# Performance work log

Measured on AMD Instinct MI355X. Metric: run time of the kernel, lower is better.

The kernel has to match this reference:

```python
import jax, jax.numpy as jnp
import numpy as np

XBOUND = (-30.0, 30.0, 0.25)
YBOUND = (-15.0, 15.0, 0.25)
ZBOUND = (-1.0, 1.0, 0.5)
EPS = 1e-9


def _heights():
    n = int((ZBOUND[1] - ZBOUND[0]) // ZBOUND[2]) + 1
    return [ZBOUND[0] + i * ZBOUND[2] for i in range(n)]


def _bev_planes():
    # matches construct_plane_grid: linspace endpoints included, meshgrid(y, x) 'ij'
    num_x = int((XBOUND[1] - XBOUND[0]) / XBOUND[2])
    num_y = int((YBOUND[1] - YBOUND[0]) / YBOUND[2])
    x = jnp.linspace(XBOUND[0], XBOUND[1], num_x, dtype=jnp.float32)
    y = jnp.linspace(YBOUND[0], YBOUND[1], num_y, dtype=jnp.float32)
    yy, xx = jnp.meshgrid(y, x, indexing='ij')
    planes = [jnp.stack([xx, yy, jnp.full_like(xx, h)], axis=-1) for h in _heights()]
    return jnp.stack(planes)  # (nlvl, bH, bW, 3)


def _bilinear_grid_sample(im, grid):
    # faithful port of the manual pad+floor+gather grid_sample (align_corners=False)
    n, c, h, w = im.shape
    gh, gw = grid.shape[1], grid.shape[2]
    x = ((grid[..., 0] + 1) * w - 1) / 2
    y = ((grid[..., 1] + 1) * h - 1) / 2
    x = x.reshape(n, -1)
    y = y.reshape(n, -1)
    x0 = jnp.floor(x)
    y0 = jnp.floor(y)
    wa = ((x0 + 1 - x) * (y0 + 1 - y))[:, None, :]
    wb = ((x0 + 1 - x) * (y - y0))[:, None, :]
    wc = ((x - x0) * (y0 + 1 - y))[:, None, :]
    wd = ((x - x0) * (y - y0))[:, None, :]
    pw, ph = w + 2, h + 2
    # clip in float first to avoid int32 overflow; out-of-range lands on zero padding either way
    x0f = jnp.clip(x0, -2.0, w + 2.0)
    y0f = jnp.clip(y0, -2.0, h + 2.0)
    x0i = jnp.clip(x0f.astype(jnp.int32) + 1, 0, pw - 1)
    x1i = jnp.clip(x0f.astype(jnp.int32) + 2, 0, pw - 1)
    y0i = jnp.clip(y0f.astype(jnp.int32) + 1, 0, ph - 1)
    y1i = jnp.clip(y0f.astype(jnp.int32) + 2, 0, ph - 1)
    im_flat = jnp.pad(im, ((0, 0), (0, 0), (1, 1), (1, 1))).reshape(n, c, -1)

    def gather(xi, yi):
        return jnp.take_along_axis(im_flat, (xi + yi * pw)[:, None, :], axis=2)

    out = (gather(x0i, y0i) * wa + gather(x0i, y1i) * wb
           + gather(x1i, y0i) * wc + gather(x1i, y1i) * wd)
    return out.reshape(n, c, gh, gw)


def _campos(pts, ego2cam, img_h, img_w):
    # pts: (B, q, 3); ego2cam: (B, ncam, 4, 4)
    B, q, _ = pts.shape
    ncam = ego2cam.shape[1]
    pts_h = jnp.concatenate([pts, jnp.ones_like(pts[..., :1])], axis=-1)  # (B,q,4)
    cam = jnp.einsum('bnij,bqj->bnqi', ego2cam, pts_h)  # (B,ncam,q,4)
    z = cam[..., 2:3]
    mask = z > EPS
    xy = cam[..., 0:2] / z + EPS
    px = xy[..., 0:1] / img_w
    py = xy[..., 1:2] / img_h
    p = (jnp.concatenate([px, py], axis=-1) - 0.5) * 2
    mask = (mask & (p[..., 0:1] > -1.0) & (p[..., 0:1] < 1.0)
            & (p[..., 1:2] > -1.0) & (p[..., 1:2] < 1.0))
    return p.reshape(B * ncam, q, 2), mask.reshape(B, ncam, q)


def reference(cam_feat, ego2cam, conv_w, conv_b, img_h, img_w):
    B, ncam = ego2cam.shape[0], ego2cam.shape[1]
    C = cam_feat.shape[1]
    planes = _bev_planes().astype(cam_feat.dtype)  # (nlvl,bH,bW,3)
    nlvl, bH, bW, _ = planes.shape
    pts = jnp.broadcast_to(planes.reshape(1, -1, 3), (B, nlvl * bH * bW, 3))
    pos, mask = _campos(pts, ego2cam, img_h, img_w)
    grid = pos.reshape(B * ncam, nlvl * bH, bW, 2)
    proj = _bilinear_grid_sample(cam_feat, grid).reshape(B, ncam, C, nlvl, bH, bW)
    m = mask.reshape(B, ncam, 1, nlvl, bH, bW).astype(proj.dtype)
    feat = (proj * m).sum(axis=1)            # (B,C,nlvl,bH,bW)
    num = m.sum(axis=1)                      # (B,1,nlvl,bH,bW)
    feat = feat / jnp.where(num == 0, jnp.ones_like(num), num)
    coords = jnp.broadcast_to(jnp.transpose(planes, (3, 0, 1, 2))[None], (B, 3, nlvl, bH, bW))
    feat = jnp.concatenate([feat, coords], axis=1).reshape(B, (C + 3) * nlvl, bH, bW)
    out = jax.lax.conv_general_dilated(
        feat, conv_w, window_strides=(1, 1), padding=((1, 1), (1, 1)),
        dimension_numbers=('NCHW', 'OIHW', 'NCHW'))
    return out + conv_b[None, :, None, None]


def setup_inputs() -> dict:
    key = jax.random.key(0)
    k1, k2, k3 = jax.random.split(key, 3)
    B, ncam, C = 1, 6, 128
    cH, cW = 64, 176
    nlvl = 5
    cam_feat = jax.random.normal(k1, (B * ncam, C, cH, cW), dtype=jnp.float32)
    ego2cam = jax.random.normal(k2, (B, ncam, 4, 4), dtype=jnp.float32)
    conv_w = jax.random.normal(k3, (128, (C + 3) * nlvl, 3, 3), dtype=jnp.float32) * 0.02
    conv_b = jnp.zeros((128,), dtype=jnp.float32)
    return {'cam_feat': cam_feat, 'ego2cam': ego2cam, 'conv_w': conv_w,
            'conv_b': conv_b, 'img_h': 512, 'img_w': 1408}
```

## Files before the change

### kernel.cpp

```cpp
#include <hip/hip_runtime.h>
#include <hip/hip_bf16.h>

#define BH 120
#define BW 240
#define NLVL 5
#define NCAM 6
#define CH 128
#define FH 64
#define FW 176
#define CIN 655
#define CINP 672
#define NCT 21
#define FROWS 124
#define FCOLS 242
#define NPIX (BH*BW)

typedef __hip_bfloat16 bf16;
typedef __attribute__((ext_vector_type(8))) short s16x8;
typedef __attribute__((ext_vector_type(4))) float f32x4;

#define G_AS __attribute__((address_space(1)))
#define L_AS __attribute__((address_space(3)))

__device__ __forceinline__ float bf2f(unsigned short u) {
    union { unsigned int i; float f; } c; c.i = ((unsigned int)u) << 16; return c.f;
}

__global__ __launch_bounds__(256) void transpose_kernel(
    const float* __restrict__ in, float* __restrict__ out)
{
    __shared__ float t[32][129];
    int n = blockIdx.z, h = blockIdx.y, w0 = blockIdx.x * 32;
    int wlim = min(32, FW - w0);
    int wx = threadIdx.x & 31, cg = threadIdx.x >> 5;
    if (wx < wlim) {
        #pragma unroll
        for (int k = 0; k < 16; ++k) {
            int c = cg + k * 8;
            t[wx][c] = in[((n*CH + c)*FH + h)*FW + w0 + wx];
        }
    }
    __syncthreads();
    int c2 = threadIdx.x & 127, wi = threadIdx.x >> 7;
    for (int w = wi; w < wlim; w += 2)
        out[((n*FH + h)*FW + w0 + w)*CH + c2] = t[w][c2];
}

__global__ __launch_bounds__(256) void wprep_kernel(
    const float* __restrict__ w, bf16* __restrict__ wbf)
{
    int idx = blockIdx.x * 256 + threadIdx.x;
    if (idx >= 128 * CINP) return;
    int oc = idx / CINP, cin = idx - oc * CINP;
    float v[9];
    if (cin < CIN) {
        const float* s = w + ((size_t)oc * CIN + cin) * 9;
        #pragma unroll
        for (int k = 0; k < 9; ++k) v[k] = s[k];
    } else {
        #pragma unroll
        for (int k = 0; k < 9; ++k) v[k] = 0.f;
    }
    #pragma unroll
    for (int k = 0; k < 9; ++k)
        wbf[(size_t)(k * 128 + oc) * CINP + cin] = __float2bfloat16(v[k]);
}

__global__ __launch_bounds__(128) void border_kernel(bf16* __restrict__ feat)
{
    int b = blockIdx.x;
    int row, col;
    if (b < 242)      { row = 0;   col = b; }
    else if (b < 484) { row = 121; col = b - 242; }
    else if (b < 604) { row = b - 484 + 1; col = 0; }
    else              { row = b - 604 + 1; col = 241; }
    s16x8* p = (s16x8*)(feat + ((size_t)row*FCOLS + col)*CINP);
    int t = threadIdx.x;
    if (t < 84) p[t] = (s16x8){0,0,0,0,0,0,0,0};
}

__global__ __launch_bounds__(128) void proj_kernel(
    const float* __restrict__ camt,
    const float* __restrict__ e2c,
    const int* __restrict__ pimgh, const int* __restrict__ pimgw,
    bf16* __restrict__ feat)
{
    __shared__ float sfx[30], sfy[30];
    __shared__ int   six[30], siy[30], svalid[30];

    int pix = blockIdx.x;
    int bx = pix % BW, by = pix / BW;
    float xw = (float)(-30.0 + bx * (60.0/239.0)); if (bx == BW-1) xw = 30.f;
    float yw = (float)(-15.0 + by * (30.0/119.0)); if (by == BH-1) yw = 15.f;

    int t = threadIdx.x;
    if (t < 30) {
        int l = t / 6, cam = t % 6;
        float h = -1.f + 0.5f * (float)l;
        const float* M = e2c + cam * 16;
        float cx = M[0]*xw + M[1]*yw + M[2]*h  + M[3];
        float cy = M[4]*xw + M[5]*yw + M[6]*h  + M[7];
        float cz = M[8]*xw + M[9]*yw + M[10]*h + M[11];
        float fw = (float)pimgw[0], fh = (float)pimgh[0];
        float px = ((cx/cz + 1e-9f)/fw - 0.5f) * 2.f;
        float py = ((cy/cz + 1e-9f)/fh - 0.5f) * 2.f;
        bool valid = (cz > 1e-9f) && (px > -1.f) && (px < 1.f)
                                  && (py > -1.f) && (py < 1.f);
        float xs = ((px + 1.f)*(float)FW - 1.f) * 0.5f;
        float ys = ((py + 1.f)*(float)FH - 1.f) * 0.5f;
        float x0 = floorf(xs), y0 = floorf(ys);
        sfx[t] = xs - x0;  sfy[t] = ys - y0;
        six[t] = (int)x0;  siy[t] = (int)y0;
        svalid[t] = valid ? 1 : 0;
    }
    __syncthreads();

    int c = t;
    float vals[NLVL];
    #pragma unroll
    for (int l = 0; l < NLVL; ++l) {
        float acc = 0.f; int cnt = 0;
        #pragma unroll
        for (int cam = 0; cam < NCAM; ++cam) {
            int id = l*6 + cam;
            if (svalid[id]) {
                int ix = six[id], iy = siy[id];
                float fx = sfx[id], fy = sfy[id];
                const float* bp = camt + (((size_t)cam*FH + iy)*FW + ix)*CH + c;
                float v00 = (ix >= 0    && iy >= 0   ) ? bp[0]        : 0.f;
                float v01 = (ix >= 0    && iy <  FH-1) ? bp[FW*CH]    : 0.f;
                float v10 = (ix <  FW-1 && iy >= 0   ) ? bp[CH]       : 0.f;
                float v11 = (ix <  FW-1 && iy <  FH-1) ? bp[FW*CH+CH] : 0.f;
                acc += (1.f-fx)*(1.f-fy)*v00 + (1.f-fx)*fy*v01
                     +      fx *(1.f-fy)*v10 +      fx *fy*v11;
                cnt++;
            }
        }
        vals[l] = acc / (float)(cnt > 0 ? cnt : 1);
    }

    bf16* dst = feat + ((size_t)(by+1)*FCOLS + (bx+1))*CINP;
    #pragma unroll
    for (int l = 0; l < NLVL; ++l)
        dst[c*5 + l] = __float2bfloat16(vals[l]);
    if (t < 15) {
        int j = t / 5, l = t % 5;
        float v = (j == 0) ? xw : (j == 1) ? yw : (-1.f + 0.5f*(float)l);
        dst[(CH + j)*5 + l] = __float2bfloat16(v);
    }
}

__global__ __launch_bounds__(256, 4) void conv_mfma_kernel(
    const bf16* __restrict__ feat,
    const bf16* __restrict__ wbf,
    bf16* __restrict__ part)
{
    __shared__ __align__(16) char lds[40960];
    const int tid  = threadIdx.x;
    const int wv   = tid >> 6;
    const int lane = tid & 63;
    const int t15  = tid & 15;
    const int kgl  = (tid >> 4) & 3;
    const int y0p = blockIdx.y * 8;
    const int x0p = blockIdx.x * 16;
    const int q   = blockIdx.z;
    const int ct0 = q ? (1 + 5*q) : 0;
    const int nph = (q ? 5 : 6) * 9;

    const int HB0 = 0, HB1 = 12288, WB0 = 24576, WB1 = 32768;

    f32x4 acc[8][2];
    #pragma unroll
    for (int m = 0; m < 8; ++m)
        #pragma unroll
        for (int f = 0; f < 2; ++f)
            acc[m][f] = (f32x4){0.f, 0.f, 0.f, 0.f};

    auto stageW = [&](int ct, int off, int wb) {
        #pragma unroll
        for (int jj = 0; jj < 2; ++jj) {
            int j = 2*wv + jj;
            int cch = j*64 + lane;
            int oc = cch >> 2, kgp = cch & 3;
            int kg = kgp ^ ((oc >> 1) & 3);
            const bf16* src = wbf + ((size_t)(off*128 + oc)*CINP + ct*32 + kg*8);
            __builtin_amdgcn_global_load_lds((const G_AS void*)src,
                                             (L_AS void*)(lds + wb + j*1024),
                                             16, 0, 0);
        }
    };
    auto stageH = [&](int ct, int hb) {
        #pragma unroll
        for (int kk = 0; kk < 3; ++kk) {
            int j = wv + 4*kk;
            int cch = j*64 + lane;
            int pp = cch >> 2, kgp = cch & 3;
            int kg = kgp ^ ((pp >> 1) & 3);
            int row = pp / 18;
            int col = pp - row*18;
            const bf16* src = feat + ((size_t)(y0p + row)*FCOLS + (x0p + col))*CINP
                                   + ct*32 + kg*8;
            __builtin_amdgcn_global_load_lds((const G_AS void*)src,
                                             (L_AS void*)(lds + hb + j*1024),
                                             16, 0, 0);
        }
    };

    stageH(ct0, HB0);
    stageW(ct0, 0, WB0);
    __syncthreads();

    int lct = 0, off = 0;
    for (int p = 0; p < nph; ++p) {
        if (p + 1 < nph) {
            int off1 = off + 1, lct1 = lct;
            if (off1 == 9) { off1 = 0; ++lct1; }
            stageW(ct0 + lct1, off1, ((p+1) & 1) ? WB1 : WB0);
            if (off1 == 0) stageH(ct0 + lct1, (lct1 & 1) ? HB1 : HB0);
        }
        const int wb = (p & 1) ? WB1 : WB0;
        const int hb = (lct & 1) ? HB1 : HB0;
        const int ky = off / 3, kx = off - ky*3;

        s16x8 A[8];
        #pragma unroll
        for (int m = 0; m < 8; ++m) {
            int oc = m*16 + t15;
            A[m] = *(const s16x8*)(lds + wb + oc*64 + ((kgl ^ ((oc>>1)&3)) << 4));
        }
        #pragma unroll
        for (int f = 0; f < 2; ++f) {
            int prow = (2*wv + f + ky)*18 + t15 + kx;
            s16x8 Bv = *(const s16x8*)(lds + hb + prow*64 + ((kgl ^ ((prow>>1)&3)) << 4));
            __builtin_amdgcn_s_setprio(1);
            #pragma unroll
            for (int m = 0; m < 8; ++m)
                acc[m][f] = __builtin_amdgcn_mfma_f32_16x16x32_bf16(A[m], Bv, acc[m][f], 0, 0, 0);
            __builtin_amdgcn_s_setprio(0);
        }
        __syncthreads();
        if (++off == 9) { off = 0; ++lct; }
    }

    bf16* pq = part + (size_t)q * (128*NPIX);
    const int xo = x0p + t15;
    #pragma unroll
    for (int m = 0; m < 8; ++m) {
        #pragma unroll
        for (int r = 0; r < 4; ++r) {
            int oc = m*16 + kgl*4 + r;
            #pragma unroll
            for (int f = 0; f < 2; ++f) {
                int y = y0p + 2*wv + f;
                pq[(size_t)oc*NPIX + y*BW + xo] = __float2bfloat16(acc[m][f][r]);
            }
        }
    }
}

__global__ __launch_bounds__(256) void combine_kernel(
    const bf16* __restrict__ part, const float* __restrict__ bias,
    float* __restrict__ out)
{
    int i8 = blockIdx.x * 256 + threadIdx.x;
    if (i8 >= 128*NPIX/8) return;
    int oc = i8 / (NPIX/8);
    float s[8];
    float b = bias[oc];
    #pragma unroll
    for (int k = 0; k < 8; ++k) s[k] = b;
    #pragma unroll
    for (int qq = 0; qq < 4; ++qq) {
        s16x8 v = *(const s16x8*)(part + (size_t)qq*(128*NPIX) + (size_t)i8*8);
        #pragma unroll
        for (int k = 0; k < 8; ++k) s[k] += bf2f((unsigned short)v[k]);
    }
    f32x4* o = (f32x4*)(out + (size_t)i8*8);
    o[0] = (f32x4){s[0], s[1], s[2], s[3]};
    o[1] = (f32x4){s[4], s[5], s[6], s[7]};
}

extern "C" void kernel_launch(void* const* d_in, const int* in_sizes, int n_in,
                              void* d_out, int out_size, void* d_ws, size_t ws_size,
                              hipStream_t stream)
{
    const float* cam_feat = (const float*)d_in[0];
    const float* ego2cam  = (const float*)d_in[1];
    const float* conv_w   = (const float*)d_in[2];
    const float* conv_b   = (const float*)d_in[3];
    const int*   img_h    = (const int*)d_in[4];
    const int*   img_w    = (const int*)d_in[5];
    float* out = (float*)d_out;

    float* camt = (float*)d_ws;
    bf16* feat = (bf16*)(camt + (size_t)NCAM*CH*FH*FW);
    bf16* wbf  = feat + (size_t)FROWS*FCOLS*CINP;
    bf16* part = (bf16*)d_ws;

    transpose_kernel<<<dim3(6, FH, NCAM), 256, 0, stream>>>(cam_feat, camt);
    wprep_kernel<<<(128*CINP + 255)/256, 256, 0, stream>>>(conv_w, wbf);
    border_kernel<<<724, 128, 0, stream>>>(feat);
    proj_kernel<<<NPIX, 128, 0, stream>>>(camt, ego2cam, img_h, img_w, feat);
    conv_mfma_kernel<<<dim3(15, 15, 4), 256, 0, stream>>>(feat, wbf, part);
    combine_kernel<<<(128*NPIX/8 + 255)/256, 256, 0, stream>>>(part, conv_b, out);
}
```

Measured before the change: 123.5 us.

## Restructure projection kernel: wave per pixel, float2 gathers, packed bf16 stores

The projection kernel now handles four BEV pixels per 256-thread block, one wave per pixel, and each lane covers two channels. Bilinear corner indices are clamped and folded into precomputed per-sample weights that already include the 1/count averaging. That removes per-corner bounds branches and lets each lane read corners with float2 loads. The five-level outputs for both channels are packed into one 16-byte store plus one 4-byte store instead of ten scalar bf16 stores. The cost is a second block barrier and more shared-memory setup, and the edge-case weight folding must reproduce zero-padding semantics exactly.

```diff
diff --git a/kernel.cpp b/kernel.cpp
--- a/kernel.cpp
+++ b/kernel.cpp
@@ -18,12 +18,18 @@
 typedef __hip_bfloat16 bf16;
 typedef __attribute__((ext_vector_type(8))) short s16x8;
 typedef __attribute__((ext_vector_type(4))) float f32x4;
+typedef __attribute__((ext_vector_type(2))) float f32x2;
+typedef unsigned int uint;
+typedef __attribute__((ext_vector_type(4), aligned(4))) uint uint4a;
 
 #define G_AS __attribute__((address_space(1)))
 #define L_AS __attribute__((address_space(3)))
 
 __device__ __forceinline__ float bf2f(unsigned short u) {
     union { unsigned int i; float f; } c; c.i = ((unsigned int)u) << 16; return c.f;
+}
+__device__ __forceinline__ uint f2bu(float x) {
+    return (uint)__hip_bfloat16_raw(__float2bfloat16(x)).x;
 }
 
 __global__ __launch_bounds__(256) void transpose_kernel(
@@ -79,74 +85,108 @@
     if (t < 84) p[t] = (s16x8){0,0,0,0,0,0,0,0};
 }
 
-__global__ __launch_bounds__(128) void proj_kernel(
+__global__ __launch_bounds__(256) void proj_kernel(
     const float* __restrict__ camt,
     const float* __restrict__ e2c,
     const int* __restrict__ pimgh, const int* __restrict__ pimgw,
     bf16* __restrict__ feat)
 {
-    __shared__ float sfx[30], sfy[30];
-    __shared__ int   six[30], siy[30], svalid[30];
-
-    int pix = blockIdx.x;
-    int bx = pix % BW, by = pix / BW;
+    __shared__ int   s_soff[4][32];
+    __shared__ float s_w4[4][30][4];
+    __shared__ int   s_val[4][32];
+
+    const int wv = threadIdx.x >> 6;
+    const int lane = threadIdx.x & 63;
+    const int pix = blockIdx.x * 4 + wv;
+    const int bx = pix % BW, by = pix / BW;
     float xw = (float)(-30.0 + bx * (60.0/239.0)); if (bx == BW-1) xw = 30.f;
     float yw = (float)(-15.0 + by * (30.0/119.0)); if (by == BH-1) yw = 15.f;
 
-    int t = threadIdx.x;
-    if (t < 30) {
-        int l = t / 6, cam = t % 6;
+    const bool act = lane < 30;
+    int valid = 0, ix = 0, iy = 0, cam = 0;
+    float fx = 0.f, fy = 0.f;
+    if (act) {
+        int l = lane / 6; cam = lane - l*6;
         float h = -1.f + 0.5f * (float)l;
         const float* M = e2c + cam * 16;
         float cx = M[0]*xw + M[1]*yw + M[2]*h  + M[3];
         float cy = M[4]*xw + M[5]*yw + M[6]*h  + M[7];
         float cz = M[8]*xw + M[9]*yw + M[10]*h + M[11];
-        float fw = (float)pimgw[0], fh = (float)pimgh[0];
-        float px = ((cx/cz + 1e-9f)/fw - 0.5f) * 2.f;
-        float py = ((cy/cz + 1e-9f)/fh - 0.5f) * 2.f;
-        bool valid = (cz > 1e-9f) && (px > -1.f) && (px < 1.f)
-                                  && (py > -1.f) && (py < 1.f);
+        float iw = (float)pimgw[0], ih = (float)pimgh[0];
+        float px = ((cx/cz + 1e-9f)/iw - 0.5f) * 2.f;
+        float py = ((cy/cz + 1e-9f)/ih - 0.5f) * 2.f;
+        valid = (cz > 1e-9f) && (px > -1.f) && (px < 1.f)
+                             && (py > -1.f) && (py < 1.f);
         float xs = ((px + 1.f)*(float)FW - 1.f) * 0.5f;
         float ys = ((py + 1.f)*(float)FH - 1.f) * 0.5f;
         float x0 = floorf(xs), y0 = floorf(ys);
-        sfx[t] = xs - x0;  sfy[t] = ys - y0;
-        six[t] = (int)x0;  siy[t] = (int)y0;
-        svalid[t] = valid ? 1 : 0;
+        fx = xs - x0; fy = ys - y0;
+        ix = (int)x0; iy = (int)y0;
+        s_val[wv][lane] = valid;
     }
     __syncthreads();
-
-    int c = t;
-    float vals[NLVL];
+    if (act) {
+        int lbase = (lane / 6) * 6;
+        int cnt = s_val[wv][lbase] + s_val[wv][lbase+1] + s_val[wv][lbase+2]
+                + s_val[wv][lbase+3] + s_val[wv][lbase+4] + s_val[wv][lbase+5];
+        float inv = (cnt > 0) ? (1.f / (float)cnt) : 0.f;
+        float sc = valid ? inv : 0.f;
+        int bx0 = min(max(ix, 0), FW-2);
+        int by0 = min(max(iy, 0), FH-2);
+        float gx0 = (1.f - fx) * sc, gx1 = fx * sc;
+        float wx0 = 0.f, wx1 = 0.f;
+        if (ix >= 0)     { if (ix == bx0) wx0 += gx0; else wx1 += gx0; }
+        if (ix+1 <= FW-1){ if (ix+1 == bx0) wx0 += gx1; else wx1 += gx1; }
+        float wy0 = 0.f, wy1 = 0.f;
+        float gy0 = 1.f - fy, gy1 = fy;
+        if (iy >= 0)     { if (iy == by0) wy0 += gy0; else wy1 += gy0; }
+        if (iy+1 <= FH-1){ if (iy+1 == by0) wy0 += gy1; else wy1 += gy1; }
+        s_w4[wv][lane][0] = wx0 * wy0;
+        s_w4[wv][lane][1] = wx0 * wy1;
+        s_w4[wv][lane][2] = wx1 * wy0;
+        s_w4[wv][lane][3] = wx1 * wy1;
+        s_soff[wv][lane] = valid ? ((cam*FH + by0)*FW + bx0)*CH : -1;
+    }
+    __syncthreads();
+
+    const int c2 = lane * 2;
+    float va[NLVL], vb[NLVL];
+    #pragma unroll
+    for (int l = 0; l < NLVL; ++l) { va[l] = 0.f; vb[l] = 0.f; }
+
     #pragma unroll
     for (int l = 0; l < NLVL; ++l) {
-        float acc = 0.f; int cnt = 0;
-        #pragma unroll
-        for (int cam = 0; cam < NCAM; ++cam) {
-            int id = l*6 + cam;
-            if (svalid[id]) {
-                int ix = six[id], iy = siy[id];
-                float fx = sfx[id], fy = sfy[id];
-                const float* bp = camt + (((size_t)cam*FH + iy)*FW + ix)*CH + c;
-                float v00 = (ix >= 0    && iy >= 0   ) ? bp[0]        : 0.f;
-                float v01 = (ix >= 0    && iy <  FH-1) ? bp[FW*CH]    : 0.f;
-                float v10 = (ix <  FW-1 && iy >= 0   ) ? bp[CH]       : 0.f;
-                float v11 = (ix <  FW-1 && iy <  FH-1) ? bp[FW*CH+CH] : 0.f;
-                acc += (1.f-fx)*(1.f-fy)*v00 + (1.f-fx)*fy*v01
-                     +      fx *(1.f-fy)*v10 +      fx *fy*v11;
-                cnt++;
+        #pragma unroll
+        for (int cm = 0; cm < NCAM; ++cm) {
+            int id = l*6 + cm;
+            int so = s_soff[wv][id];
+            if (so >= 0) {
+                const float* bp = camt + so + c2;
+                f32x2 t0 = *(const f32x2*)(bp);
+                f32x2 t2 = *(const f32x2*)(bp + CH);
+                f32x2 t1 = *(const f32x2*)(bp + FW*CH);
+                f32x2 t3 = *(const f32x2*)(bp + FW*CH + CH);
+                float w0 = s_w4[wv][id][0], w1 = s_w4[wv][id][1];
+                float w2 = s_w4[wv][id][2], w3 = s_w4[wv][id][3];
+                va[l] += w0*t0[0] + w1*t1[0] + w2*t2[0] + w3*t3[0];
+                vb[l] += w0*t0[1] + w1*t1[1] + w2*t2[1] + w3*t3[1];
             }
         }
-        vals[l] = acc / (float)(cnt > 0 ? cnt : 1);
-    }
-
-    bf16* dst = feat + ((size_t)(by+1)*FCOLS + (bx+1))*CINP;
-    #pragma unroll
-    for (int l = 0; l < NLVL; ++l)
-        dst[c*5 + l] = __float2bfloat16(vals[l]);
-    if (t < 15) {
-        int j = t / 5, l = t % 5;
+    }
+
+    bf16* dpix = feat + ((size_t)(by+1)*FCOLS + (bx+1))*CINP;
+    uint u0 = f2bu(va[0]) | (f2bu(va[1]) << 16);
+    uint u1 = f2bu(va[2]) | (f2bu(va[3]) << 16);
+    uint u2 = f2bu(va[4]) | (f2bu(vb[0]) << 16);
+    uint u3 = f2bu(vb[1]) | (f2bu(vb[2]) << 16);
+    uint u4 = f2bu(vb[3]) | (f2bu(vb[4]) << 16);
+    char* dst = (char*)(dpix + c2*5);
+    *(uint4a*)dst = (uint4a){u0, u1, u2, u3};
+    *(uint*)(dst + 16) = u4;
+    if (lane < 15) {
+        int j = lane / 5, l = lane - j*5;
         float v = (j == 0) ? xw : (j == 1) ? yw : (-1.f + 0.5f*(float)l);
-        dst[(CH + j)*5 + l] = __float2bfloat16(v);
+        dpix[CH*5 + lane] = __float2bfloat16(v);
     }
 }
 
@@ -300,7 +340,7 @@
     transpose_kernel<<<dim3(6, FH, NCAM), 256, 0, stream>>>(cam_feat, camt);
     wprep_kernel<<<(128*CINP + 255)/256, 256, 0, stream>>>(conv_w, wbf);
     border_kernel<<<724, 128, 0, stream>>>(feat);
-    proj_kernel<<<NPIX, 128, 0, stream>>>(camt, ego2cam, img_h, img_w, feat);
+    proj_kernel<<<NPIX/4, 256, 0, stream>>>(camt, ego2cam, img_h, img_w, feat);
     conv_mfma_kernel<<<dim3(15, 15, 4), 256, 0, stream>>>(feat, wbf, part);
     combine_kernel<<<(128*NPIX/8 + 255)/256, 256, 0, stream>>>(part, conv_b, out);
 }
```

Result: faster. 118.8 us (-3.8%).
